# Kernel optimization log

Hardware: AMD Instinct MI355X
Metric: run time of the kernel (lower is better)

## Reference

```python
import jax, jax.numpy as jnp
import numpy as np

N_NODES = 100000
N_EDGES = 1000000
D_IN = 64
D_OUT = 64


def setup_inputs() -> dict:
    key = jax.random.key(0)
    k_x, k_e, k_wl, k_bl, k_wr = jax.random.split(key, 5)
    x = jax.random.normal(k_x, (N_NODES, D_IN), dtype=jnp.float32)
    edge_index = jax.random.randint(k_e, (2, N_EDGES), 0, N_NODES, dtype=jnp.int64)
    scale = 1.0 / np.sqrt(D_IN)
    # SAGEConv params: lin_l (neighbor path, with bias), lin_r (root/self path, no bias)
    W_l = jax.random.uniform(k_wl, (D_OUT, D_IN), dtype=jnp.float32, minval=-scale, maxval=scale)
    b_l = jax.random.uniform(k_bl, (D_OUT,), dtype=jnp.float32, minval=-scale, maxval=scale)
    W_r = jax.random.uniform(k_wr, (D_OUT, D_IN), dtype=jnp.float32, minval=-scale, maxval=scale)
    return {"x": x, "edge_index": edge_index, "W_l": W_l, "b_l": b_l, "W_r": W_r}


def reference(x, edge_index, W_l, b_l, W_r):
    # PyG SAGEConv with mean aggregation:
    #   out = lin_l(mean_{j in N(i)} x_j) + lin_r(x_i);  then ReLU (from GCN.forward)
    src = edge_index[0]  # message sources
    dst = edge_index[1]  # aggregation targets
    n = x.shape[0]
    msg = x[src]  # [E, D_IN] gather
    agg = jax.ops.segment_sum(msg, dst, num_segments=n)  # [N, D_IN]
    deg = jax.ops.segment_sum(jnp.ones((src.shape[0],), x.dtype), dst, num_segments=n)
    mean = agg / jnp.maximum(deg, 1.0)[:, None]  # isolated nodes -> 0
    out = mean @ W_l.T + b_l + x @ W_r.T
    return jax.nn.relu(out)
```

## Files before the change

kernel.cpp:

```cpp
#include <hip/hip_runtime.h>

#define N_NODES 100000
#define N_EDGES 1000000
#define D 64

#define NFINE 782
#define CAP2 1536
#define CHUNK 4096
#define EDGE_BLOCKS 245
#define CONV_BLOCKS 6250
#define CONS_BLOCKS 3128
#define STR 132
#define SCAP 512

typedef unsigned short u16;
typedef unsigned int u32;
using bf16x8 = __attribute__((ext_vector_type(8))) short;
using f32x4  = __attribute__((ext_vector_type(4))) float;

__device__ __forceinline__ u16 f2bf(float f) {
    u32 u = __float_as_uint(f);
    return (u16)((u + 0x7FFF + ((u >> 16) & 1)) >> 16);
}
__device__ __forceinline__ float bf2f(u16 v) {
    return __uint_as_float(((u32)v) << 16);
}

__global__ __launch_bounds__(256) void conv_zero_kernel(
    const float* __restrict__ x, u16* __restrict__ xb,
    int* __restrict__ cur2,
    const float* __restrict__ Wl, const float* __restrict__ Wr,
    u16* __restrict__ Wb) {
    if (blockIdx.x == CONV_BLOCKS) {
        for (int j = threadIdx.x; j < NFINE; j += 256) cur2[j] = 0;
        return;
    }
    if (blockIdx.x == CONV_BLOCKS + 1) {
        int o = threadIdx.x >> 2;
        int k0 = (threadIdx.x & 3) * 32;
        const float4* wlf = (const float4*)Wl;
        const float4* wrf = (const float4*)Wr;
        #pragma unroll
        for (int j = 0; j < 8; j++) {
            int k = k0 + j * 4;
            float4 v = (k < 64) ? wlf[(o * 64 + k) >> 2]
                                : wrf[(o * 64 + k - 64) >> 2];
            *(ushort4*)&Wb[o * 128 + k] =
                make_ushort4(f2bf(v.x), f2bf(v.y), f2bf(v.z), f2bf(v.w));
        }
        return;
    }
    int i = blockIdx.x * 256 + threadIdx.x;
    float4 v = ((const float4*)x)[i];
    ((ushort4*)xb)[i] = make_ushort4(f2bf(v.x), f2bf(v.y), f2bf(v.z), f2bf(v.w));
}

__global__ __launch_bounds__(1024) void build3_kernel(
    const int* __restrict__ ei, int* __restrict__ cur2,
    u32* __restrict__ pairs2) {
    __shared__ u32 sorted[CHUNK];
    __shared__ u16 binof[CHUNK];
    __shared__ int hist[NFINE];
    __shared__ int off_l[NFINE];
    __shared__ int cur_l[NFINE];
    __shared__ int base_g[NFINE];
    __shared__ int wsum[16];

    int b = blockIdx.x;
    int t = threadIdx.x;
    int ln = t & 63;
    int wv = t >> 6;

    const u32* uu = (const u32*)ei;
    int f = 1;
    #pragma unroll
    for (int i = 1; i < 16; i += 2)
        if (uu[i] != 0u) f = 0;

    if (t < NFINE) hist[t] = 0;
    __syncthreads();

    int e0 = b * CHUNK;
    int e1 = min(e0 + CHUNK, N_EDGES);
    int ne = e1 - e0;

    const uint2* e64 = (const uint2*)ei;
    int srcv[4], dstv[4];
    #pragma unroll
    for (int i = 0; i < 4; i++) {
        int ee = e0 + t + i * 1024;
        bool ok = ee < e1;
        if (f) {
            uint2 sv = ok ? e64[ee] : make_uint2(0u, 0u);
            uint2 dv = ok ? e64[N_EDGES + ee] : make_uint2(0u, 0u);
            srcv[i] = (int)sv.x;
            dstv[i] = ok ? (int)dv.x : -1;
        } else {
            srcv[i] = ok ? ei[ee] : 0;
            dstv[i] = ok ? ei[N_EDGES + ee] : -1;
        }
    }
    #pragma unroll
    for (int i = 0; i < 4; i++)
        if (dstv[i] >= 0) atomicAdd(&hist[dstv[i] >> 7], 1);
    __syncthreads();

    int h = (t < NFINE) ? hist[t] : 0;
    int inc = h;
    #pragma unroll
    for (int o = 1; o < 64; o <<= 1) {
        int v = __shfl_up(inc, o);
        if (ln >= o) inc += v;
    }
    if (ln == 63) wsum[wv] = inc;
    __syncthreads();
    if (t < 16) {
        int w = wsum[t];
        int winc = w;
        #pragma unroll
        for (int o = 1; o < 16; o <<= 1) {
            int v = __shfl_up(winc, o);
            if (t >= o) winc += v;
        }
        wsum[t] = winc - w;
    }
    __syncthreads();
    if (t < NFINE) {
        int ex = inc - h + wsum[wv];
        off_l[t] = ex;
        cur_l[t] = ex;
        base_g[t] = h ? atomicAdd(&cur2[t], h) : 0;
    }
    __syncthreads();

    #pragma unroll
    for (int i = 0; i < 4; i++) {
        if (dstv[i] >= 0) {
            int fine = dstv[i] >> 7;
            int slot = atomicAdd(&cur_l[fine], 1);
            sorted[slot] = (u32)srcv[i] | ((u32)(dstv[i] & 127) << 17);
            binof[slot] = (u16)fine;
        }
    }
    __syncthreads();

    for (int i = t; i < ne; i += 1024) {
        int fine = binof[i];
        int pos = base_g[fine] + (i - off_l[fine]);
        if (pos < CAP2)
            pairs2[(size_t)fine * CAP2 + pos] = sorted[i];
    }
}

__global__ __launch_bounds__(256) void cons7_kernel(
    const u16* __restrict__ xb, const u16* __restrict__ Wb,
    const float* __restrict__ bl,
    const int* __restrict__ cur2, const u32* __restrict__ pairs2,
    float* __restrict__ out) {
    __shared__ u16 As[32 * STR];
    __shared__ int sorted_s[SCAP];
    __shared__ int deg_l[32];
    __shared__ int off_l[32];
    __shared__ int cur_l[32];

    int tid = threadIdx.x;
    int bin = blockIdx.x >> 2;
    int quarter = blockIdx.x & 3;
    int nbase = bin * 128 + quarter * 32;
    if (nbase >= N_NODES) return;

    int lane = tid & 63;
    int wv = tid >> 6;

    int cnt = min(cur2[bin], CAP2);
    const u32* pb = &pairs2[(size_t)bin * CAP2];
    u32 ve[6];
    #pragma unroll
    for (int i = 0; i < 6; i++) {
        int e = tid + i * 256;
        ve[i] = (e < cnt) ? pb[e] : 0xFFFFFFFFu;
    }

    if (tid < 32) { deg_l[tid] = 0; cur_l[tid] = 0; }
    if (tid == 0) sorted_s[0] = 0;
    __syncthreads();

    #pragma unroll
    for (int i = 0; i < 6; i++) {
        u32 v = ve[i];
        if ((int)(v >> 22) == quarter) atomicAdd(&deg_l[(v >> 17) & 31], 1);
    }
    __syncthreads();

    if (tid < 32) {
        int dd = deg_l[tid];
        int inc = dd;
        #pragma unroll
        for (int o = 1; o < 32; o <<= 1) {
            int v = __shfl_up(inc, o);
            if (tid >= o) inc += v;
        }
        off_l[tid] = inc - dd;
    }
    __syncthreads();

    #pragma unroll
    for (int i = 0; i < 6; i++) {
        u32 v = ve[i];
        if ((int)(v >> 22) == quarter) {
            int lnn = (v >> 17) & 31;
            int p = off_l[lnn] + atomicAdd(&cur_l[lnn], 1);
            if (p < SCAP) sorted_s[p] = (int)(v & 0x1FFFFu);
        }
    }
    __syncthreads();

    int nl8 = lane >> 3;
    int c = lane & 7;
    int nl = wv * 8 + nl8;
    int n = nbase + nl;
    int d = deg_l[nl];
    int st = off_l[nl];

    int maxd = d;
    maxd = max(maxd, __shfl_xor(maxd, 8));
    maxd = max(maxd, __shfl_xor(maxd, 16));
    maxd = max(maxd, __shfl_xor(maxd, 32));

    float acc[8];
    #pragma unroll
    for (int j = 0; j < 8; j++) acc[j] = 0.0f;

    int dm1 = (d > 0) ? (d - 1) : 0;
    int sb = (d > 0) ? st : 0;
    for (int k = 0; k < maxd; k += 8) {
        int ix[8];
        #pragma unroll
        for (int u = 0; u < 8; u++) ix[u] = sb + min(k + u, dm1);
        int s0 = sorted_s[ix[0]];
        int s1 = sorted_s[ix[1]];
        int s2 = sorted_s[ix[2]];
        int s3 = sorted_s[ix[3]];
        int s4 = sorted_s[ix[4]];
        int s5 = sorted_s[ix[5]];
        int s6 = sorted_s[ix[6]];
        int s7 = sorted_s[ix[7]];
        bf16x8 r0 = *(const bf16x8*)&xb[(size_t)s0 * D + c * 8];
        bf16x8 r1 = *(const bf16x8*)&xb[(size_t)s1 * D + c * 8];
        bf16x8 r2 = *(const bf16x8*)&xb[(size_t)s2 * D + c * 8];
        bf16x8 r3 = *(const bf16x8*)&xb[(size_t)s3 * D + c * 8];
        bf16x8 r4 = *(const bf16x8*)&xb[(size_t)s4 * D + c * 8];
        bf16x8 r5 = *(const bf16x8*)&xb[(size_t)s5 * D + c * 8];
        bf16x8 r6 = *(const bf16x8*)&xb[(size_t)s6 * D + c * 8];
        bf16x8 r7 = *(const bf16x8*)&xb[(size_t)s7 * D + c * 8];
        float m0 = (k + 0 < d) ? 1.0f : 0.0f;
        float m1 = (k + 1 < d) ? 1.0f : 0.0f;
        float m2 = (k + 2 < d) ? 1.0f : 0.0f;
        float m3 = (k + 3 < d) ? 1.0f : 0.0f;
        float m4 = (k + 4 < d) ? 1.0f : 0.0f;
        float m5 = (k + 5 < d) ? 1.0f : 0.0f;
        float m6 = (k + 6 < d) ? 1.0f : 0.0f;
        float m7 = (k + 7 < d) ? 1.0f : 0.0f;
        #pragma unroll
        for (int j = 0; j < 8; j++) acc[j] = fmaf(m0, bf2f((u16)r0[j]), acc[j]);
        #pragma unroll
        for (int j = 0; j < 8; j++) acc[j] = fmaf(m1, bf2f((u16)r1[j]), acc[j]);
        #pragma unroll
        for (int j = 0; j < 8; j++) acc[j] = fmaf(m2, bf2f((u16)r2[j]), acc[j]);
        #pragma unroll
        for (int j = 0; j < 8; j++) acc[j] = fmaf(m3, bf2f((u16)r3[j]), acc[j]);
        #pragma unroll
        for (int j = 0; j < 8; j++) acc[j] = fmaf(m4, bf2f((u16)r4[j]), acc[j]);
        #pragma unroll
        for (int j = 0; j < 8; j++) acc[j] = fmaf(m5, bf2f((u16)r5[j]), acc[j]);
        #pragma unroll
        for (int j = 0; j < 8; j++) acc[j] = fmaf(m6, bf2f((u16)r6[j]), acc[j]);
        #pragma unroll
        for (int j = 0; j < 8; j++) acc[j] = fmaf(m7, bf2f((u16)r7[j]), acc[j]);
    }

    int mtile = wv >> 1;
    int nt0 = (wv & 1) * 2;
    int lrow = lane & 15;
    int quad = lane >> 4;

    const u16* wb0 = &Wb[((nt0 + 0) * 16 + lrow) * 128 + quad * 8];
    const u16* wb1 = &Wb[((nt0 + 1) * 16 + lrow) * 128 + quad * 8];
    bf16x8 bf0_0 = *(const bf16x8*)&wb0[0 * 32];
    bf16x8 bf0_1 = *(const bf16x8*)&wb0[1 * 32];
    bf16x8 bf0_2 = *(const bf16x8*)&wb0[2 * 32];
    bf16x8 bf0_3 = *(const bf16x8*)&wb0[3 * 32];
    bf16x8 bf1_0 = *(const bf16x8*)&wb1[0 * 32];
    bf16x8 bf1_1 = *(const bf16x8*)&wb1[1 * 32];
    bf16x8 bf1_2 = *(const bf16x8*)&wb1[2 * 32];
    bf16x8 bf1_3 = *(const bf16x8*)&wb1[3 * 32];

    float inv = (d > 0) ? (1.0f / (float)d) : 0.0f;
    bf16x8 p;
    #pragma unroll
    for (int j = 0; j < 8; j++) p[j] = (short)f2bf(acc[j] * inv);
    *(bf16x8*)&As[nl * STR + c * 8] = p;
    bf16x8 xr = {0, 0, 0, 0, 0, 0, 0, 0};
    if (n < N_NODES) xr = *(const bf16x8*)&xb[(size_t)n * D + c * 8];
    *(bf16x8*)&As[nl * STR + 64 + c * 8] = xr;
    __syncthreads();

    const u16* Ab = &As[(mtile * 16 + lrow) * STR + quad * 8];

    float bias0 = bl[(nt0 + 0) * 16 + lrow];
    float bias1 = bl[(nt0 + 1) * 16 + lrow];
    f32x4 acc0 = {bias0, bias0, bias0, bias0};
    f32x4 acc1 = {bias1, bias1, bias1, bias1};

    {
        bf16x8 af;
        af = *(const bf16x8*)&Ab[0 * 32];
        acc0 = __builtin_amdgcn_mfma_f32_16x16x32_bf16(af, bf0_0, acc0, 0, 0, 0);
        acc1 = __builtin_amdgcn_mfma_f32_16x16x32_bf16(af, bf1_0, acc1, 0, 0, 0);
        af = *(const bf16x8*)&Ab[1 * 32];
        acc0 = __builtin_amdgcn_mfma_f32_16x16x32_bf16(af, bf0_1, acc0, 0, 0, 0);
        acc1 = __builtin_amdgcn_mfma_f32_16x16x32_bf16(af, bf1_1, acc1, 0, 0, 0);
        af = *(const bf16x8*)&Ab[2 * 32];
        acc0 = __builtin_amdgcn_mfma_f32_16x16x32_bf16(af, bf0_2, acc0, 0, 0, 0);
        acc1 = __builtin_amdgcn_mfma_f32_16x16x32_bf16(af, bf1_2, acc1, 0, 0, 0);
        af = *(const bf16x8*)&Ab[3 * 32];
        acc0 = __builtin_amdgcn_mfma_f32_16x16x32_bf16(af, bf0_3, acc0, 0, 0, 0);
        acc1 = __builtin_amdgcn_mfma_f32_16x16x32_bf16(af, bf1_3, acc1, 0, 0, 0);
    }

    int node = nbase + mtile * 16 + quad * 4;
    #pragma unroll
    for (int r = 0; r < 4; r++) {
        if (node + r < N_NODES) {
            out[(size_t)(node + r) * D + (nt0 + 0) * 16 + lrow] = fmaxf(acc0[r], 0.0f);
            out[(size_t)(node + r) * D + (nt0 + 1) * 16 + lrow] = fmaxf(acc1[r], 0.0f);
        }
    }
}

extern "C" void kernel_launch(void* const* d_in, const int* in_sizes, int n_in,
                              void* d_out, int out_size, void* d_ws, size_t ws_size,
                              hipStream_t stream) {
    const float* x  = (const float*)d_in[0];
    const int*   ei = (const int*)d_in[1];
    const float* Wl = (const float*)d_in[2];
    const float* bl = (const float*)d_in[3];
    const float* Wr = (const float*)d_in[4];
    float* out = (float*)d_out;

    char* p = (char*)d_ws;
    int* cur2   = (int*)p;                        p += 1024 * sizeof(int);
    u16* Wb     = (u16*)p;                        p += 8192 * sizeof(u16);
    u32* pairs2 = (u32*)p;                        p += (size_t)NFINE * CAP2 * sizeof(u32);
    u16* xb     = (u16*)p;

    conv_zero_kernel<<<CONV_BLOCKS + 2, 256, 0, stream>>>(x, xb, cur2, Wl, Wr, Wb);
    build3_kernel<<<EDGE_BLOCKS, 1024, 0, stream>>>(ei, cur2, pairs2);
    cons7_kernel<<<CONS_BLOCKS, 256, 0, stream>>>(xb, Wb, bl, cur2, pairs2, out);
}
```

Baseline: 130.8 us.

## Fuse bf16 conversion of x and weights into edge-binning kernel

Removes the separate conversion/zeroing kernel. The x-to-bf16 conversion and the weight packing now run inside the edge-binning kernel, with each thread prefetching seven float4s alongside its edge loads. Zeroing of the bin counters moves to a hipMemsetAsync, and the global bin counters are padded to 16-int stride to cut atomic contention and false sharing. The aim is to save a kernel launch and overlap conversion traffic with binning. In exchange, the binning kernel holds more registers and does more work per block.

```diff
diff --git a/kernel.cpp b/kernel.cpp
--- a/kernel.cpp
+++ b/kernel.cpp
@@ -8,10 +8,12 @@
 #define CAP2 1536
 #define CHUNK 4096
 #define EDGE_BLOCKS 245
-#define CONV_BLOCKS 6250
+#define CONV_ITEMS 1600000
+#define CONV_STRIDE (EDGE_BLOCKS * 1024)
 #define CONS_BLOCKS 3128
 #define STR 132
 #define SCAP 512
+#define CSTR 16
 
 typedef unsigned short u16;
 typedef unsigned int u32;
@@ -26,36 +28,10 @@
     return __uint_as_float(((u32)v) << 16);
 }
 
-__global__ __launch_bounds__(256) void conv_zero_kernel(
+__global__ __launch_bounds__(1024) void build5_kernel(
     const float* __restrict__ x, u16* __restrict__ xb,
-    int* __restrict__ cur2,
     const float* __restrict__ Wl, const float* __restrict__ Wr,
-    u16* __restrict__ Wb) {
-    if (blockIdx.x == CONV_BLOCKS) {
-        for (int j = threadIdx.x; j < NFINE; j += 256) cur2[j] = 0;
-        return;
-    }
-    if (blockIdx.x == CONV_BLOCKS + 1) {
-        int o = threadIdx.x >> 2;
-        int k0 = (threadIdx.x & 3) * 32;
-        const float4* wlf = (const float4*)Wl;
-        const float4* wrf = (const float4*)Wr;
-        #pragma unroll
-        for (int j = 0; j < 8; j++) {
-            int k = k0 + j * 4;
-            float4 v = (k < 64) ? wlf[(o * 64 + k) >> 2]
-                                : wrf[(o * 64 + k - 64) >> 2];
-            *(ushort4*)&Wb[o * 128 + k] =
-                make_ushort4(f2bf(v.x), f2bf(v.y), f2bf(v.z), f2bf(v.w));
-        }
-        return;
-    }
-    int i = blockIdx.x * 256 + threadIdx.x;
-    float4 v = ((const float4*)x)[i];
-    ((ushort4*)xb)[i] = make_ushort4(f2bf(v.x), f2bf(v.y), f2bf(v.z), f2bf(v.w));
-}
-
-__global__ __launch_bounds__(1024) void build3_kernel(
+    u16* __restrict__ Wb,
     const int* __restrict__ ei, int* __restrict__ cur2,
     u32* __restrict__ pairs2) {
     __shared__ u32 sorted[CHUNK];
@@ -100,6 +76,30 @@
             dstv[i] = ok ? ei[N_EDGES + ee] : -1;
         }
     }
+
+    float4 cf[7];
+    const float4* x4 = (const float4*)x;
+    #pragma unroll
+    for (int j = 0; j < 7; j++) {
+        int i = b * 1024 + t + j * CONV_STRIDE;
+        cf[j] = (i < CONV_ITEMS) ? x4[i] : make_float4(0.f, 0.f, 0.f, 0.f);
+    }
+
+    if (b == 0 && t < 256) {
+        int o = t >> 2;
+        int k0 = (t & 3) * 32;
+        const float4* wlf = (const float4*)Wl;
+        const float4* wrf = (const float4*)Wr;
+        #pragma unroll
+        for (int j = 0; j < 8; j++) {
+            int k = k0 + j * 4;
+            float4 v = (k < 64) ? wlf[(o * 64 + k) >> 2]
+                                : wrf[(o * 64 + k - 64) >> 2];
+            *(ushort4*)&Wb[o * 128 + k] =
+                make_ushort4(f2bf(v.x), f2bf(v.y), f2bf(v.z), f2bf(v.w));
+        }
+    }
+
     #pragma unroll
     for (int i = 0; i < 4; i++)
         if (dstv[i] >= 0) atomicAdd(&hist[dstv[i] >> 7], 1);
@@ -125,11 +125,22 @@
         wsum[t] = winc - w;
     }
     __syncthreads();
+
     if (t < NFINE) {
         int ex = inc - h + wsum[wv];
         off_l[t] = ex;
         cur_l[t] = ex;
-        base_g[t] = h ? atomicAdd(&cur2[t], h) : 0;
+        base_g[t] = h ? atomicAdd(&cur2[t * CSTR], h) : 0;
+    }
+
+    #pragma unroll
+    for (int j = 0; j < 7; j++) {
+        int i = b * 1024 + t + j * CONV_STRIDE;
+        if (i < CONV_ITEMS) {
+            float4 v = cf[j];
+            ((ushort4*)xb)[i] =
+                make_ushort4(f2bf(v.x), f2bf(v.y), f2bf(v.z), f2bf(v.w));
+        }
     }
     __syncthreads();
 
@@ -172,7 +183,7 @@
     int lane = tid & 63;
     int wv = tid >> 6;
 
-    int cnt = min(cur2[bin], CAP2);
+    int cnt = min(cur2[bin * CSTR], CAP2);
     const u32* pb = &pairs2[(size_t)bin * CAP2];
     u32 ve[6];
     #pragma unroll
@@ -349,12 +360,12 @@
     float* out = (float*)d_out;
 
     char* p = (char*)d_ws;
-    int* cur2   = (int*)p;                        p += 1024 * sizeof(int);
+    int* cur2   = (int*)p;                        p += (size_t)NFINE * CSTR * sizeof(int);
     u16* Wb     = (u16*)p;                        p += 8192 * sizeof(u16);
     u32* pairs2 = (u32*)p;                        p += (size_t)NFINE * CAP2 * sizeof(u32);
     u16* xb     = (u16*)p;
 
-    conv_zero_kernel<<<CONV_BLOCKS + 2, 256, 0, stream>>>(x, xb, cur2, Wl, Wr, Wb);
-    build3_kernel<<<EDGE_BLOCKS, 1024, 0, stream>>>(ei, cur2, pairs2);
+    hipMemsetAsync(cur2, 0, (size_t)NFINE * CSTR * sizeof(int), stream);
+    build5_kernel<<<EDGE_BLOCKS, 1024, 0, stream>>>(x, xb, Wl, Wr, Wb, ei, cur2, pairs2);
     cons7_kernel<<<CONS_BLOCKS, 256, 0, stream>>>(xb, Wb, bl, cur2, pairs2, out);
 }
```

Measured after the change: 134.2 us. 2.6% more time.

## Scatter edges directly to global bins and pad bin counters to separate lines

Applied to the files above, without the earlier changes.

The build kernel no longer runs a block-local prefix scan and a shared-memory staging sort. Each edge now takes a local slot with a shared atomic and writes straight to its global bin position. The global per-bin counters are padded by a stride of 16 ints so each sits on its own 64-byte region, which is meant to reduce atomic contention and false sharing between neighbouring bins. The trade-off is less coalesced global writes, because the scattered stores are no longer grouped by bin. The padding also enlarges the counter array that has to be zeroed.

```diff
diff --git a/kernel.cpp b/kernel.cpp
--- a/kernel.cpp
+++ b/kernel.cpp
@@ -12,6 +12,7 @@
 #define CONS_BLOCKS 3128
 #define STR 132
 #define SCAP 512
+#define CSTR 16
 
 typedef unsigned short u16;
 typedef unsigned int u32;
@@ -32,7 +33,7 @@
     const float* __restrict__ Wl, const float* __restrict__ Wr,
     u16* __restrict__ Wb) {
     if (blockIdx.x == CONV_BLOCKS) {
-        for (int j = threadIdx.x; j < NFINE; j += 256) cur2[j] = 0;
+        for (int j = threadIdx.x; j < NFINE * CSTR; j += 256) cur2[j] = 0;
         return;
     }
     if (blockIdx.x == CONV_BLOCKS + 1) {
@@ -55,21 +56,15 @@
     ((ushort4*)xb)[i] = make_ushort4(f2bf(v.x), f2bf(v.y), f2bf(v.z), f2bf(v.w));
 }
 
-__global__ __launch_bounds__(1024) void build3_kernel(
+__global__ __launch_bounds__(1024) void build6_kernel(
     const int* __restrict__ ei, int* __restrict__ cur2,
     u32* __restrict__ pairs2) {
-    __shared__ u32 sorted[CHUNK];
-    __shared__ u16 binof[CHUNK];
     __shared__ int hist[NFINE];
-    __shared__ int off_l[NFINE];
     __shared__ int cur_l[NFINE];
     __shared__ int base_g[NFINE];
-    __shared__ int wsum[16];
 
     int b = blockIdx.x;
     int t = threadIdx.x;
-    int ln = t & 63;
-    int wv = t >> 6;
 
     const u32* uu = (const u32*)ei;
     int f = 1;
@@ -77,12 +72,11 @@
     for (int i = 1; i < 16; i += 2)
         if (uu[i] != 0u) f = 0;
 
-    if (t < NFINE) hist[t] = 0;
+    if (t < NFINE) { hist[t] = 0; cur_l[t] = 0; }
     __syncthreads();
 
     int e0 = b * CHUNK;
     int e1 = min(e0 + CHUNK, N_EDGES);
-    int ne = e1 - e0;
 
     const uint2* e64 = (const uint2*)ei;
     int srcv[4], dstv[4];
@@ -105,31 +99,9 @@
         if (dstv[i] >= 0) atomicAdd(&hist[dstv[i] >> 7], 1);
     __syncthreads();
 
-    int h = (t < NFINE) ? hist[t] : 0;
-    int inc = h;
-    #pragma unroll
-    for (int o = 1; o < 64; o <<= 1) {
-        int v = __shfl_up(inc, o);
-        if (ln >= o) inc += v;
-    }
-    if (ln == 63) wsum[wv] = inc;
-    __syncthreads();
-    if (t < 16) {
-        int w = wsum[t];
-        int winc = w;
-        #pragma unroll
-        for (int o = 1; o < 16; o <<= 1) {
-            int v = __shfl_up(winc, o);
-            if (t >= o) winc += v;
-        }
-        wsum[t] = winc - w;
-    }
-    __syncthreads();
     if (t < NFINE) {
-        int ex = inc - h + wsum[wv];
-        off_l[t] = ex;
-        cur_l[t] = ex;
-        base_g[t] = h ? atomicAdd(&cur2[t], h) : 0;
+        int h = hist[t];
+        base_g[t] = h ? atomicAdd(&cur2[t * CSTR], h) : 0;
     }
     __syncthreads();
 
@@ -137,18 +109,12 @@
     for (int i = 0; i < 4; i++) {
         if (dstv[i] >= 0) {
             int fine = dstv[i] >> 7;
-            int slot = atomicAdd(&cur_l[fine], 1);
-            sorted[slot] = (u32)srcv[i] | ((u32)(dstv[i] & 127) << 17);
-            binof[slot] = (u16)fine;
-        }
-    }
-    __syncthreads();
-
-    for (int i = t; i < ne; i += 1024) {
-        int fine = binof[i];
-        int pos = base_g[fine] + (i - off_l[fine]);
-        if (pos < CAP2)
-            pairs2[(size_t)fine * CAP2 + pos] = sorted[i];
+            int loc = atomicAdd(&cur_l[fine], 1);
+            int pos = base_g[fine] + loc;
+            if (pos < CAP2)
+                pairs2[(size_t)fine * CAP2 + pos] =
+                    (u32)srcv[i] | ((u32)(dstv[i] & 127) << 17);
+        }
     }
 }
 
@@ -172,7 +138,7 @@
     int lane = tid & 63;
     int wv = tid >> 6;
 
-    int cnt = min(cur2[bin], CAP2);
+    int cnt = min(cur2[bin * CSTR], CAP2);
     const u32* pb = &pairs2[(size_t)bin * CAP2];
     u32 ve[6];
     #pragma unroll
@@ -349,12 +315,12 @@
     float* out = (float*)d_out;
 
     char* p = (char*)d_ws;
-    int* cur2   = (int*)p;                        p += 1024 * sizeof(int);
+    int* cur2   = (int*)p;                        p += (size_t)NFINE * CSTR * sizeof(int);
     u16* Wb     = (u16*)p;                        p += 8192 * sizeof(u16);
     u32* pairs2 = (u32*)p;                        p += (size_t)NFINE * CAP2 * sizeof(u32);
     u16* xb     = (u16*)p;
 
     conv_zero_kernel<<<CONV_BLOCKS + 2, 256, 0, stream>>>(x, xb, cur2, Wl, Wr, Wb);
-    build3_kernel<<<EDGE_BLOCKS, 1024, 0, stream>>>(ei, cur2, pairs2);
+    build6_kernel<<<EDGE_BLOCKS, 1024, 0, stream>>>(ei, cur2, pairs2);
     cons7_kernel<<<CONS_BLOCKS, 256, 0, stream>>>(xb, Wb, bl, cur2, pairs2, out);
 }
```

After: 138.1 us. 5.6% more time.
